# Kernel tuning notes

Measured on AMD Instinct MI355X. Metric: run time of the kernel, lower is better.

Reference implementation:

```python
import jax, jax.numpy as jnp
import numpy as np

LOW_THRESH, HIGH_THRESH = 0.1, 0.2   # kornia canny defaults
HYST_ITERS = 10                      # fixed-point hysteresis iterations (fixed for jit)


def _gaussian_kernel5(sigma=1.0):
    x = jnp.arange(5, dtype=jnp.float32) - 2.0
    g = jnp.exp(-0.5 * (x / sigma) ** 2)
    g = g / g.sum()
    return jnp.outer(g, g)  # [5,5]


def _conv2d(x, k):
    # x: [B,1,H,W]; k: [kh,kw]; reflect pad + VALID conv == SAME with reflect border
    kh, kw = k.shape
    xp = jnp.pad(x, ((0, 0), (0, 0), (kh // 2, kh // 2), (kw // 2, kw // 2)), mode="reflect")
    return jax.lax.conv_general_dilated(
        xp, k[None, None], (1, 1), "VALID",
        dimension_numbers=("NCHW", "OIHW", "NCHW"))


def _shift(x, dy, dx):
    # value of neighbor at (i+dy, j+dx), zero-padded border; x: [B,1,H,W]
    H, W = x.shape[2], x.shape[3]
    xp = jnp.pad(x, ((0, 0), (0, 0), (1, 1), (1, 1)))
    return xp[:, :, 1 + dy:1 + dy + H, 1 + dx:1 + dx + W]


def _canny_edges(img):
    # img: [B,3,H,W] in [0,1] -> binary edge map [B,1,H,W]
    gray = 0.299 * img[:, :1] + 0.587 * img[:, 1:2] + 0.114 * img[:, 2:3]
    blur = _conv2d(gray, _gaussian_kernel5())
    sobel_x = jnp.array([[-1., 0., 1.], [-2., 0., 2.], [-1., 0., 1.]], jnp.float32)
    gx = _conv2d(blur, sobel_x)
    gy = _conv2d(blur, sobel_x.T)
    mag = jnp.sqrt(gx * gx + gy * gy + 1e-12)
    ang = jnp.arctan2(gy, gx)

    # non-maximum suppression: quantize gradient direction to 4 bins (0/45/90/135 deg)
    b = jnp.mod(jnp.round(ang / (jnp.pi / 4.0)), 4).astype(jnp.int32)  # [B,1,H,W]
    n_pos = jnp.stack([_shift(mag, 0, 1), _shift(mag, 1, 1),
                       _shift(mag, 1, 0), _shift(mag, 1, -1)], axis=0)  # [4,B,1,H,W]
    n_neg = jnp.stack([_shift(mag, 0, -1), _shift(mag, -1, -1),
                       _shift(mag, -1, 0), _shift(mag, -1, 1)], axis=0)
    n1 = jnp.take_along_axis(n_pos, b[None], axis=0)[0]
    n2 = jnp.take_along_axis(n_neg, b[None], axis=0)[0]
    nms = jnp.where((mag >= n1) & (mag >= n2), mag, 0.0)

    # double threshold: strong=1.0, weak=0.5
    edges = jnp.where(nms >= HIGH_THRESH, 1.0,
                      jnp.where(nms >= LOW_THRESH, 0.5, 0.0))

    # hysteresis: weak pixels with a strong 8-neighbor become strong (iterated)
    def body(_, e):
        strong = (e == 1.0).astype(e.dtype)
        nb = jax.lax.reduce_window(strong, 0.0, jax.lax.max,
                                   (1, 1, 3, 3), (1, 1, 1, 1), "SAME")
        promoted = (e == 0.5) & (nb > 0.5)
        return jnp.where(promoted, 1.0, e)

    edges = jax.lax.fori_loop(0, HYST_ITERS, body, edges)
    return (edges == 1.0).astype(jnp.float32)


def setup_inputs() -> dict:
    key = jax.random.key(0)
    k1, k2 = jax.random.split(key)
    shape = (16, 3, 512, 512)
    return {"y_hat": jax.random.uniform(k1, shape, jnp.float32),
            "y": jax.random.uniform(k2, shape, jnp.float32)}


def reference(y_hat, y):
    y_hat_edges = _canny_edges(y_hat)
    y_edges = _canny_edges(y)
    return jnp.mean(jnp.abs(y_hat_edges - y_edges))  # F.l1_loss, mean reduction
```

## Files before the change

kernel.cpp:

```cpp
#include <hip/hip_runtime.h>
#include <math.h>

#define H 512
#define W 512
#define IMG (H*W)
#define NIMG 32

typedef unsigned long long u64;

__device__ __forceinline__ int reflect_idx(int i, int n) {
    if (i < 0) i = -i;
    if (i >= n) i = 2 * n - 2 - i;
    return i;
}

#define EBX 64
#define EBY 16

__global__ __launch_bounds__(512) void k_edges(const float* __restrict__ yhat,
                                               const float* __restrict__ yy,
                                               u64* __restrict__ strongP,
                                               u64* __restrict__ weakP) {
    __shared__ float sg[EBY + 8][EBX + 8 + 1];
    __shared__ float ht[EBY + 8][EBX + 4 + 1];
    __shared__ float sb[EBY + 4][EBX + 4 + 1];
    __shared__ float sm[EBY + 2][EBX + 2 + 1];

    const int n = blockIdx.z;
    const float* src = (n < 16) ? (yhat + (size_t)n * 3 * IMG)
                                : (yy + (size_t)(n - 16) * 3 * IMG);
    const int x0 = blockIdx.x * EBX;
    const int y0 = blockIdx.y * EBY;
    const int tid = threadIdx.y * EBX + threadIdx.x;

    const float w0 = 0.05448868454964294f, w1 = 0.24420134200323332f,
                w2 = 0.4026199468942475f;
    const float wk[5] = {w0, w1, w2, w1, w0};

    for (int idx = tid; idx < 24 * 72; idx += 512) {
        int sy = idx / 72, sx = idx % 72;
        int iy = reflect_idx(y0 - 4 + sy, H);
        int ix = reflect_idx(x0 - 4 + sx, W);
        float r = src[(size_t)iy * W + ix];
        float g = src[(size_t)IMG + (size_t)iy * W + ix];
        float b = src[(size_t)2 * IMG + (size_t)iy * W + ix];
        sg[sy][sx] = 0.299f * r + 0.587f * g + 0.114f * b;
    }
    __syncthreads();

    for (int idx = tid; idx < 24 * 68; idx += 512) {
        int sy = idx / 68, sx = idx % 68;
        float a = 0.f;
#pragma unroll
        for (int v = 0; v < 5; v++) a += wk[v] * sg[sy][sx + v];
        ht[sy][sx] = a;
    }
    __syncthreads();

    for (int idx = tid; idx < 20 * 68; idx += 512) {
        int sy = idx / 68, sx = idx % 68;
        float a = 0.f;
#pragma unroll
        for (int u = 0; u < 5; u++) a += wk[u] * ht[sy + u][sx];
        sb[sy][sx] = a;
    }
    __syncthreads();

    for (int idx = tid; idx < 18 * 66; idx += 512) {
        int my = idx / 66, mx = idx % 66;
        int iy = y0 - 1 + my, ix = x0 - 1 + mx;
        float m = 0.f;
        if (iy >= 0 && iy < H && ix >= 0 && ix < W) {
            float a00 = sb[my][mx],     a01 = sb[my][mx + 1],     a02 = sb[my][mx + 2];
            float a10 = sb[my + 1][mx],                           a12 = sb[my + 1][mx + 2];
            float a20 = sb[my + 2][mx], a21 = sb[my + 2][mx + 1], a22 = sb[my + 2][mx + 2];
            float gx = (a02 + 2.f * a12 + a22) - (a00 + 2.f * a10 + a20);
            float gy = (a20 + 2.f * a21 + a22) - (a00 + 2.f * a01 + a02);
            m = sqrtf(gx * gx + gy * gy + 1e-12f);
        }
        sm[my][mx] = m;
    }
    __syncthreads();

    const int tx = threadIdx.x;
#pragma unroll
    for (int half = 0; half < 2; half++) {
        const int ry = threadIdx.y + half * 8;
        float a00 = sb[ry + 1][tx + 1], a01 = sb[ry + 1][tx + 2], a02 = sb[ry + 1][tx + 3];
        float a10 = sb[ry + 2][tx + 1],                           a12 = sb[ry + 2][tx + 3];
        float a20 = sb[ry + 3][tx + 1], a21 = sb[ry + 3][tx + 2], a22 = sb[ry + 3][tx + 3];
        float gx = (a02 + 2.f * a12 + a22) - (a00 + 2.f * a10 + a20);
        float gy = (a20 + 2.f * a21 + a22) - (a00 + 2.f * a01 + a02);
        float mag = sm[ry + 1][tx + 1];

        float ax = fabsf(gx), ay = fabsf(gy);
        int dy, dx;
        if (ay <= 0.4142135623730951f * ax) { dy = 0; dx = 1; }
        else if (ay >= 2.414213562373095f * ax) { dy = 1; dx = 0; }
        else { dy = 1; dx = ((gx > 0.f) == (gy > 0.f)) ? 1 : -1; }

        float n1 = sm[ry + 1 + dy][tx + 1 + dx];
        float n2 = sm[ry + 1 - dy][tx + 1 - dx];
        float nms = (mag >= n1 && mag >= n2) ? mag : 0.f;

        u64 strong = __ballot(nms >= 0.2f);
        u64 weak   = __ballot(nms >= 0.1f);
        if (tx == 0) {
            size_t off = ((size_t)n * H + (y0 + ry)) * 8 + blockIdx.x;
            strongP[off] = strong;
            weakP[off] = weak;
        }
    }
}

__device__ __forceinline__ u64 ldw(const u64* p, int img, int y, int w, bool ok) {
    return (ok && w >= 0 && w < 8) ? p[((size_t)img * H + y) * 8 + w] : 0ULL;
}

__global__ __launch_bounds__(256) void k_hyst(const u64* __restrict__ strongP,
                                              const u64* __restrict__ weakP,
                                              unsigned int* __restrict__ partials) {
    __shared__ unsigned int part[4];
    const int wy = threadIdx.x >> 6;
    const int wave = blockIdx.x * 4 + wy;
    const int lane = threadIdx.x & 63;
    const int tile = wave & 255;
    const int pair = wave >> 8;
    const int tx0 = (tile & 15) * 32;
    const int ty0 = (tile >> 4) * 32;

    const int y = ty0 - 10 + lane;
    const bool rowok = (lane < 52) && (y >= 0) && (y < H);
    const int s = tx0 - 10;
    const int w0i = s >> 6;
    const int r = s & 63;

    const int imgA = pair, imgB = pair + 16;
    u64 sA, wA, sB, wB;
    {
        u64 lo, hi;
        lo = ldw(strongP, imgA, y, w0i, rowok); hi = ldw(strongP, imgA, y, w0i + 1, rowok);
        sA = (lo >> r) | (hi << (64 - r));
        lo = ldw(weakP, imgA, y, w0i, rowok);   hi = ldw(weakP, imgA, y, w0i + 1, rowok);
        wA = (lo >> r) | (hi << (64 - r));
        lo = ldw(strongP, imgB, y, w0i, rowok); hi = ldw(strongP, imgB, y, w0i + 1, rowok);
        sB = (lo >> r) | (hi << (64 - r));
        lo = ldw(weakP, imgB, y, w0i, rowok);   hi = ldw(weakP, imgB, y, w0i + 1, rowok);
        wB = (lo >> r) | (hi << (64 - r));
    }

#pragma unroll
    for (int it = 0; it < 10; it++) {
        u64 up = __shfl_up(sA, 1), dn = __shfl_down(sA, 1);
        u64 t = up | sA | dn;
        sA |= (t | (t << 1) | (t >> 1)) & wA;
        up = __shfl_up(sB, 1); dn = __shfl_down(sB, 1);
        t = up | sB | dn;
        sB |= (t | (t << 1) | (t >> 1)) & wB;
    }

    unsigned int c = 0;
    if (lane >= 10 && lane < 42) {
        const u64 mask = ((1ULL << 42) - (1ULL << 10));
        c = (unsigned int)__popcll((sA ^ sB) & mask);
    }
#pragma unroll
    for (int off = 32; off > 0; off >>= 1) c += __shfl_down(c, off);
    if (lane == 0) part[wy] = c;
    __syncthreads();
    if (threadIdx.x == 0)
        partials[blockIdx.x] = part[0] + part[1] + part[2] + part[3];
}

__global__ __launch_bounds__(256) void k_final(const unsigned int* __restrict__ partials,
                                               float* __restrict__ out) {
    __shared__ unsigned int part[4];
    unsigned int c = 0;
    for (int i = threadIdx.x; i < 1024; i += 256) c += partials[i];
#pragma unroll
    for (int off = 32; off > 0; off >>= 1) c += __shfl_down(c, off);
    const int lane = threadIdx.x & 63;
    const int wy = threadIdx.x >> 6;
    if (lane == 0) part[wy] = c;
    __syncthreads();
    if (threadIdx.x == 0)
        out[0] = (float)(part[0] + part[1] + part[2] + part[3]) * (1.0f / 4194304.0f);
}

extern "C" void kernel_launch(void* const* d_in, const int* in_sizes, int n_in,
                              void* d_out, int out_size, void* d_ws, size_t ws_size,
                              hipStream_t stream) {
    const float* yhat = (const float*)d_in[0];
    const float* yy = (const float*)d_in[1];

    u64* strongP = (u64*)d_ws;
    u64* weakP = strongP + (size_t)NIMG * H * 8;
    unsigned int* partials = (unsigned int*)(weakP + (size_t)NIMG * H * 8);

    dim3 eblk(EBX, 8);
    dim3 egrd(W / EBX, H / EBY, NIMG);
    k_edges<<<egrd, eblk, 0, stream>>>(yhat, yy, strongP, weakP);

    k_hyst<<<1024, 256, 0, stream>>>(strongP, weakP, partials);
    k_final<<<1, 256, 0, stream>>>(partials, (float*)d_out);
}
```

Before: 153.2 us.

## Fold Gaussian blur into separable Sobel filters and enlarge edge tile

Precomputes combined Gaussian*Sobel separable 1D kernels so gradients come from two separable passes instead of blur then Sobel, removing an intermediate stage and a sync. Doubles the row tile to 32 to cut halo overhead, reuses LDS by aliasing buffers, vectorises the horizontal pass with float4 reads, and stores a precomputed NMS neighbor offset per pixel. Floating-point results may differ slightly from blur-then-Sobel ordering, which can flip threshold decisions at the margins.

```diff
diff --git a/kernel.cpp b/kernel.cpp
--- a/kernel.cpp
+++ b/kernel.cpp
@@ -14,97 +14,111 @@
     return i;
 }
 
-#define EBX 64
-#define EBY 16
+#define S0 0.05448868454964294f
+#define S1 0.35317871110251920f
+#define S2 0.94551131545035710f
+#define S3 1.29364257779496160f
+#define A1 0.05448868454964294f
+#define A2 0.24420134200323332f
+#define A3 0.34813126234460456f
+
+#define TY 32
 
 __global__ __launch_bounds__(512) void k_edges(const float* __restrict__ yhat,
                                                const float* __restrict__ yy,
                                                u64* __restrict__ strongP,
                                                u64* __restrict__ weakP) {
-    __shared__ float sg[EBY + 8][EBX + 8 + 1];
-    __shared__ float ht[EBY + 8][EBX + 4 + 1];
-    __shared__ float sb[EBY + 4][EBX + 4 + 1];
-    __shared__ float sm[EBY + 2][EBX + 2 + 1];
+    __shared__ __align__(16) char lds[12768 + 22848];
+    float (*sg)[76] = (float (*)[76])lds;
+    float (*hxy)[68][2] = (float (*)[68][2])(lds + 12768);
+    float (*sm)[68] = (float (*)[68])lds;
+    unsigned char (*sbin)[68] = (unsigned char (*)[68])(lds + 9792);
 
     const int n = blockIdx.z;
     const float* src = (n < 16) ? (yhat + (size_t)n * 3 * IMG)
                                 : (yy + (size_t)(n - 16) * 3 * IMG);
-    const int x0 = blockIdx.x * EBX;
-    const int y0 = blockIdx.y * EBY;
-    const int tid = threadIdx.y * EBX + threadIdx.x;
-
-    const float w0 = 0.05448868454964294f, w1 = 0.24420134200323332f,
-                w2 = 0.4026199468942475f;
-    const float wk[5] = {w0, w1, w2, w1, w0};
-
-    for (int idx = tid; idx < 24 * 72; idx += 512) {
-        int sy = idx / 72, sx = idx % 72;
-        int iy = reflect_idx(y0 - 4 + sy, H);
-        int ix = reflect_idx(x0 - 4 + sx, W);
-        float r = src[(size_t)iy * W + ix];
-        float g = src[(size_t)IMG + (size_t)iy * W + ix];
-        float b = src[(size_t)2 * IMG + (size_t)iy * W + ix];
-        sg[sy][sx] = 0.299f * r + 0.587f * g + 0.114f * b;
-    }
-    __syncthreads();
-
-    for (int idx = tid; idx < 24 * 68; idx += 512) {
-        int sy = idx / 68, sx = idx % 68;
-        float a = 0.f;
-#pragma unroll
-        for (int v = 0; v < 5; v++) a += wk[v] * sg[sy][sx + v];
-        ht[sy][sx] = a;
-    }
-    __syncthreads();
-
-    for (int idx = tid; idx < 20 * 68; idx += 512) {
-        int sy = idx / 68, sx = idx % 68;
-        float a = 0.f;
-#pragma unroll
-        for (int u = 0; u < 5; u++) a += wk[u] * ht[sy + u][sx];
-        sb[sy][sx] = a;
-    }
-    __syncthreads();
-
-    for (int idx = tid; idx < 18 * 66; idx += 512) {
-        int my = idx / 66, mx = idx % 66;
-        int iy = y0 - 1 + my, ix = x0 - 1 + mx;
-        float m = 0.f;
-        if (iy >= 0 && iy < H && ix >= 0 && ix < W) {
-            float a00 = sb[my][mx],     a01 = sb[my][mx + 1],     a02 = sb[my][mx + 2];
-            float a10 = sb[my + 1][mx],                           a12 = sb[my + 1][mx + 2];
-            float a20 = sb[my + 2][mx], a21 = sb[my + 2][mx + 1], a22 = sb[my + 2][mx + 2];
-            float gx = (a02 + 2.f * a12 + a22) - (a00 + 2.f * a10 + a20);
-            float gy = (a20 + 2.f * a21 + a22) - (a00 + 2.f * a01 + a02);
-            m = sqrtf(gx * gx + gy * gy + 1e-12f);
-        }
-        sm[my][mx] = m;
-    }
-    __syncthreads();
-
-    const int tx = threadIdx.x;
-#pragma unroll
-    for (int half = 0; half < 2; half++) {
-        const int ry = threadIdx.y + half * 8;
-        float a00 = sb[ry + 1][tx + 1], a01 = sb[ry + 1][tx + 2], a02 = sb[ry + 1][tx + 3];
-        float a10 = sb[ry + 2][tx + 1],                           a12 = sb[ry + 2][tx + 3];
-        float a20 = sb[ry + 3][tx + 1], a21 = sb[ry + 3][tx + 2], a22 = sb[ry + 3][tx + 3];
-        float gx = (a02 + 2.f * a12 + a22) - (a00 + 2.f * a10 + a20);
-        float gy = (a20 + 2.f * a21 + a22) - (a00 + 2.f * a01 + a02);
-        float mag = sm[ry + 1][tx + 1];
-
-        float ax = fabsf(gx), ay = fabsf(gy);
-        int dy, dx;
-        if (ay <= 0.4142135623730951f * ax) { dy = 0; dx = 1; }
-        else if (ay >= 2.414213562373095f * ax) { dy = 1; dx = 0; }
-        else { dy = 1; dx = ((gx > 0.f) == (gy > 0.f)) ? 1 : -1; }
-
-        float n1 = sm[ry + 1 + dy][tx + 1 + dx];
-        float n2 = sm[ry + 1 - dy][tx + 1 - dx];
+    const int x0 = blockIdx.x * 64;
+    const int y0 = blockIdx.y * TY;
+    const int tx = threadIdx.x, ty = threadIdx.y;
+    const int tid = ty * 64 + tx;
+
+    const int ixA = reflect_idx(x0 - 4 + tx, W);
+    const int ixB = reflect_idx(x0 + 60 + tx, W);
+#pragma unroll
+    for (int k = 0; k < 6; k++) {
+        int sy = ty + 8 * k;
+        if (sy < 42) {
+            int iy = reflect_idx(y0 - 4 + sy, H);
+            const float* row = src + iy * W;
+            float r = row[ixA], g = row[IMG + ixA], b = row[2 * IMG + ixA];
+            sg[sy][tx] = 0.299f * r + 0.587f * g + 0.114f * b;
+            if (tx < 8) {
+                float r2 = row[ixB], g2 = row[IMG + ixB], b2 = row[2 * IMG + ixB];
+                sg[sy][64 + tx] = 0.299f * r2 + 0.587f * g2 + 0.114f * b2;
+            }
+        }
+    }
+    __syncthreads();
+
+    for (int t = tid; t < 714; t += 512) {
+        int sy = t / 17, g = t % 17;
+        const float4* p = (const float4*)&sg[sy][0];
+        float4 q0 = p[g], q1 = p[g + 1], q2 = p[g + 2];
+        float w[12] = {q0.x, q0.y, q0.z, q0.w, q1.x, q1.y, q1.z, q1.w,
+                       q2.x, q2.y, q2.z, q2.w};
+#pragma unroll
+        for (int j = 0; j < 4; j++) {
+            float hx = A3 * (w[j + 4] - w[j + 2]) + A2 * (w[j + 5] - w[j + 1])
+                     + A1 * (w[j + 6] - w[j + 0]);
+            float hy = S3 * w[j + 3] + S2 * (w[j + 4] + w[j + 2])
+                     + S1 * (w[j + 5] + w[j + 1]) + S0 * (w[j + 6] + w[j + 0]);
+            *(float2*)&hxy[sy][4 * g + j][0] = make_float2(hx, hy);
+        }
+    }
+    __syncthreads();
+
+    for (int t = tid; t < 594; t += 512) {
+        int rg = t / 66, c = t % 66;
+        float hx[10], hy[10];
+#pragma unroll
+        for (int i = 0; i < 10; i++) {
+            float2 v = *(const float2*)&hxy[4 * rg + i][c][0];
+            hx[i] = v.x; hy[i] = v.y;
+        }
+        int imgcol = x0 - 1 + c;
+        bool colok = (unsigned)imgcol < (unsigned)W;
+#pragma unroll
+        for (int j = 0; j < 4; j++) {
+            int my = 4 * rg + j;
+            float gx = S3 * hx[j + 3] + S2 * (hx[j + 4] + hx[j + 2])
+                     + S1 * (hx[j + 5] + hx[j + 1]) + S0 * (hx[j + 6] + hx[j + 0]);
+            float gy = A3 * (hy[j + 4] - hy[j + 2]) + A2 * (hy[j + 5] - hy[j + 1])
+                     + A1 * (hy[j + 6] - hy[j + 0]);
+            int imgrow = y0 - 1 + my;
+            bool ok = colok && ((unsigned)imgrow < (unsigned)H);
+            float m = ok ? sqrtf(gx * gx + gy * gy + 1e-12f) : 0.f;
+            sm[my][c] = m;
+            float ax = fabsf(gx), ay = fabsf(gy);
+            int d;
+            if (ay <= 0.4142135623730951f * ax) d = 1;
+            else if (ay >= 2.414213562373095f * ax) d = 68;
+            else d = ((gx > 0.f) == (gy > 0.f)) ? 69 : 67;
+            sbin[my][c] = (unsigned char)d;
+        }
+    }
+    __syncthreads();
+
+#pragma unroll
+    for (int k = 0; k < 4; k++) {
+        int ry = ty + 8 * k;
+        const float* cp = &sm[ry + 1][tx + 1];
+        float mag = cp[0];
+        int d = sbin[ry + 1][tx + 1];
+        float n1 = cp[d];
+        float n2 = cp[-d];
         float nms = (mag >= n1 && mag >= n2) ? mag : 0.f;
-
         u64 strong = __ballot(nms >= 0.2f);
-        u64 weak   = __ballot(nms >= 0.1f);
+        u64 weak = __ballot(nms >= 0.1f);
         if (tx == 0) {
             size_t off = ((size_t)n * H + (y0 + ry)) * 8 + blockIdx.x;
             strongP[off] = strong;
@@ -197,8 +211,8 @@
     u64* weakP = strongP + (size_t)NIMG * H * 8;
     unsigned int* partials = (unsigned int*)(weakP + (size_t)NIMG * H * 8);
 
-    dim3 eblk(EBX, 8);
-    dim3 egrd(W / EBX, H / EBY, NIMG);
+    dim3 eblk(64, 8);
+    dim3 egrd(W / 64, H / TY, NIMG);
     k_edges<<<egrd, eblk, 0, stream>>>(yhat, yy, strongP, weakP);
 
     k_hyst<<<1024, 256, 0, stream>>>(strongP, weakP, partials);
```

Result: no change. 155.9 us (+1.7%).

## Rewrite edge kernel as per-wave column strips with rolling registers and fused blur-Sobel

Applied to the files above, without the earlier changes.

Replaces the shared-memory tiled edge kernel with one wave per 56-column strip that streams rows down a 32-row band. Blur and Sobel are folded into separable 7-tap filters, and the neighbour taps are exchanged across lanes with ds_bpermute. Magnitude and direction for the last three rows are kept in registers for NMS. Squared magnitude is compared against squared thresholds so the sqrt is dropped. The bitmask layout moves to 10 strips of 56 bits, so the hysteresis kernel now stitches up to three words per row, and the halo columns mean extra recomputation.

```diff
diff --git a/kernel.cpp b/kernel.cpp
--- a/kernel.cpp
+++ b/kernel.cpp
@@ -5,6 +5,10 @@
 #define W 512
 #define IMG (H*W)
 #define NIMG 32
+#define NSTRIP 10
+#define SW 56
+#define RB 32
+#define NBAND 16
 
 typedef unsigned long long u64;
 
@@ -14,107 +18,103 @@
     return i;
 }
 
-#define EBX 64
-#define EBY 16
-
-__global__ __launch_bounds__(512) void k_edges(const float* __restrict__ yhat,
+__device__ __forceinline__ float bperm_f(int addr, float v) {
+    return __int_as_float(__builtin_amdgcn_ds_bpermute(addr, __float_as_int(v)));
+}
+
+#define S0 0.05448868454964294f
+#define S1 0.35317871110251920f
+#define S2 0.94551131545035710f
+#define S3 1.29364257779496160f
+#define A1 0.05448868454964294f
+#define A2 0.24420134200323332f
+#define A3 0.34813126234460456f
+
+__global__ __launch_bounds__(256) void k_edges(const float* __restrict__ yhat,
                                                const float* __restrict__ yy,
                                                u64* __restrict__ strongP,
                                                u64* __restrict__ weakP) {
-    __shared__ float sg[EBY + 8][EBX + 8 + 1];
-    __shared__ float ht[EBY + 8][EBX + 4 + 1];
-    __shared__ float sb[EBY + 4][EBX + 4 + 1];
-    __shared__ float sm[EBY + 2][EBX + 2 + 1];
-
-    const int n = blockIdx.z;
+    const int wid = blockIdx.x * 4 + (threadIdx.x >> 6);
+    const int lane = threadIdx.x & 63;
+    const int n = wid / (NSTRIP * NBAND);
+    const int rem = wid - n * (NSTRIP * NBAND);
+    const int s = rem >> 4;
+    const int band = rem & 15;
+    const int y0 = band * RB;
     const float* src = (n < 16) ? (yhat + (size_t)n * 3 * IMG)
                                 : (yy + (size_t)(n - 16) * 3 * IMG);
-    const int x0 = blockIdx.x * EBX;
-    const int y0 = blockIdx.y * EBY;
-    const int tid = threadIdx.y * EBX + threadIdx.x;
-
-    const float w0 = 0.05448868454964294f, w1 = 0.24420134200323332f,
-                w2 = 0.4026199468942475f;
-    const float wk[5] = {w0, w1, w2, w1, w0};
-
-    for (int idx = tid; idx < 24 * 72; idx += 512) {
-        int sy = idx / 72, sx = idx % 72;
-        int iy = reflect_idx(y0 - 4 + sy, H);
-        int ix = reflect_idx(x0 - 4 + sx, W);
-        float r = src[(size_t)iy * W + ix];
-        float g = src[(size_t)IMG + (size_t)iy * W + ix];
-        float b = src[(size_t)2 * IMG + (size_t)iy * W + ix];
-        sg[sy][sx] = 0.299f * r + 0.587f * g + 0.114f * b;
-    }
-    __syncthreads();
-
-    for (int idx = tid; idx < 24 * 68; idx += 512) {
-        int sy = idx / 68, sx = idx % 68;
-        float a = 0.f;
-#pragma unroll
-        for (int v = 0; v < 5; v++) a += wk[v] * sg[sy][sx + v];
-        ht[sy][sx] = a;
-    }
-    __syncthreads();
-
-    for (int idx = tid; idx < 20 * 68; idx += 512) {
-        int sy = idx / 68, sx = idx % 68;
-        float a = 0.f;
-#pragma unroll
-        for (int u = 0; u < 5; u++) a += wk[u] * ht[sy + u][sx];
-        sb[sy][sx] = a;
-    }
-    __syncthreads();
-
-    for (int idx = tid; idx < 18 * 66; idx += 512) {
-        int my = idx / 66, mx = idx % 66;
-        int iy = y0 - 1 + my, ix = x0 - 1 + mx;
-        float m = 0.f;
-        if (iy >= 0 && iy < H && ix >= 0 && ix < W) {
-            float a00 = sb[my][mx],     a01 = sb[my][mx + 1],     a02 = sb[my][mx + 2];
-            float a10 = sb[my + 1][mx],                           a12 = sb[my + 1][mx + 2];
-            float a20 = sb[my + 2][mx], a21 = sb[my + 2][mx + 1], a22 = sb[my + 2][mx + 2];
-            float gx = (a02 + 2.f * a12 + a22) - (a00 + 2.f * a10 + a20);
-            float gy = (a20 + 2.f * a21 + a22) - (a00 + 2.f * a01 + a02);
-            m = sqrtf(gx * gx + gy * gy + 1e-12f);
-        }
-        sm[my][mx] = m;
-    }
-    __syncthreads();
-
-    const int tx = threadIdx.x;
-#pragma unroll
-    for (int half = 0; half < 2; half++) {
-        const int ry = threadIdx.y + half * 8;
-        float a00 = sb[ry + 1][tx + 1], a01 = sb[ry + 1][tx + 2], a02 = sb[ry + 1][tx + 3];
-        float a10 = sb[ry + 2][tx + 1],                           a12 = sb[ry + 2][tx + 3];
-        float a20 = sb[ry + 3][tx + 1], a21 = sb[ry + 3][tx + 2], a22 = sb[ry + 3][tx + 3];
-        float gx = (a02 + 2.f * a12 + a22) - (a00 + 2.f * a10 + a20);
-        float gy = (a20 + 2.f * a21 + a22) - (a00 + 2.f * a01 + a02);
-        float mag = sm[ry + 1][tx + 1];
-
-        float ax = fabsf(gx), ay = fabsf(gy);
-        int dy, dx;
-        if (ay <= 0.4142135623730951f * ax) { dy = 0; dx = 1; }
-        else if (ay >= 2.414213562373095f * ax) { dy = 1; dx = 0; }
-        else { dy = 1; dx = ((gx > 0.f) == (gy > 0.f)) ? 1 : -1; }
-
-        float n1 = sm[ry + 1 + dy][tx + 1 + dx];
-        float n2 = sm[ry + 1 - dy][tx + 1 - dx];
-        float nms = (mag >= n1 && mag >= n2) ? mag : 0.f;
-
-        u64 strong = __ballot(nms >= 0.2f);
-        u64 weak   = __ballot(nms >= 0.1f);
-        if (tx == 0) {
-            size_t off = ((size_t)n * H + (y0 + ry)) * 8 + blockIdx.x;
-            strongP[off] = strong;
-            weakP[off] = weak;
-        }
-    }
-}
-
-__device__ __forceinline__ u64 ldw(const u64* p, int img, int y, int w, bool ok) {
-    return (ok && w >= 0 && w < 8) ? p[((size_t)img * H + y) * 8 + w] : 0ULL;
+
+    const int c = s * SW - 4 + lane;
+    const int cx = reflect_idx(c, W);
+    const bool colok = ((unsigned)c < (unsigned)W);
+    const u64 omask = (s == 9) ? 0xFFull : 0x00FFFFFFFFFFFFFFull;
+
+    const int aM3 = ((lane - 3) << 2), aM2 = ((lane - 2) << 2), aM1 = ((lane - 1) << 2);
+    const int aP1 = ((lane + 1) << 2), aP2 = ((lane + 2) << 2), aP3 = ((lane + 3) << 2);
+
+    float hx[7], hy[7];
+    float mPrev = 0.f, mPrevL = 0.f, mPrevR = 0.f;
+    float mCur = 0.f, mCurL = 0.f, mCurR = 0.f;
+    int dCur = 0, dNew = 0;
+
+    u64 outBase = ((size_t)n * NSTRIP + s) * H;
+
+    for (int i = 0; i < RB + 8; i++) {
+#pragma unroll
+        for (int j = 0; j < 6; j++) { hx[j] = hx[j + 1]; hy[j] = hy[j + 1]; }
+        {
+            int gr = reflect_idx(y0 - 4 + i, H);
+            const float* p = src + (size_t)gr * W + cx;
+            float g = 0.299f * p[0] + 0.587f * p[IMG] + 0.114f * p[2 * IMG];
+            float gm1 = bperm_f(aM1, g), gp1 = bperm_f(aP1, g);
+            float gm2 = bperm_f(aM2, g), gp2 = bperm_f(aP2, g);
+            float gm3 = bperm_f(aM3, g), gp3 = bperm_f(aP3, g);
+            hx[6] = A3 * (gp1 - gm1) + A2 * (gp2 - gm2) + A1 * (gp3 - gm3);
+            hy[6] = S3 * g + S2 * (gp1 + gm1) + S1 * (gp2 + gm2) + S0 * (gp3 + gm3);
+        }
+
+        float mNew = 0.f, mNewL = 0.f, mNewR = 0.f;
+        if (i >= 6) {
+            float gx = S3 * hx[3] + S2 * (hx[4] + hx[2])
+                     + S1 * (hx[5] + hx[1]) + S0 * (hx[6] + hx[0]);
+            float gy = A3 * (hy[4] - hy[2]) + A2 * (hy[5] - hy[1])
+                     + A1 * (hy[6] - hy[0]);
+            int mr = y0 - 7 + i;
+            bool ok = colok && ((unsigned)mr < (unsigned)H);
+            mNew = ok ? (gx * gx + gy * gy + 1e-12f) : 0.f;
+            mNewL = bperm_f(aM1, mNew);
+            mNewR = bperm_f(aP1, mNew);
+            float ax = fabsf(gx), ay = fabsf(gy);
+            dNew = (ay <= 0.4142135623730951f * ax) ? 0
+                 : (ay >= 2.414213562373095f * ax) ? 2
+                 : (((gx > 0.f) == (gy > 0.f)) ? 1 : 3);
+        }
+
+        if (i >= 8) {
+            float n1 = (dCur == 0) ? mCurR : (dCur == 1) ? mNewR
+                     : (dCur == 2) ? mNew : mNewL;
+            float n2 = (dCur == 0) ? mCurL : (dCur == 1) ? mPrevL
+                     : (dCur == 2) ? mPrev : mPrevR;
+            bool okn = (mCur >= n1) && (mCur >= n2);
+            u64 bs = __ballot(okn && (mCur >= 0.04f));
+            u64 bw = __ballot(okn && (mCur >= 0.01f));
+            if (lane == 0) {
+                int t = y0 - 8 + i;
+                strongP[outBase + t] = (bs >> 4) & omask;
+                weakP[outBase + t] = (bw >> 4) & omask;
+            }
+        }
+
+        if (i >= 6) {
+            mPrev = mCur; mPrevL = mCurL; mPrevR = mCurR;
+            mCur = mNew; mCurL = mNewL; mCurR = mNewR;
+            dCur = dNew;
+        }
+    }
+}
+
+__device__ __forceinline__ u64 ldw10(const u64* p, int img, int y, int q, bool ok) {
+    return (ok && q >= 0 && q < NSTRIP) ? p[((size_t)img * NSTRIP + q) * H + y] : 0ULL;
 }
 
 __global__ __launch_bounds__(256) void k_hyst(const u64* __restrict__ strongP,
@@ -131,22 +131,35 @@
 
     const int y = ty0 - 10 + lane;
     const bool rowok = (lane < 52) && (y >= 0) && (y < H);
-    const int s = tx0 - 10;
-    const int w0i = s >> 6;
-    const int r = s & 63;
+    const int yc = rowok ? y : 0;
+
+    const int x = tx0 - 10;
+    const int q0 = (x < 0) ? -1 : (x / 56);
+    const int r = x - 56 * q0;
+    const int sh1 = 56 - r;
+    const bool need3 = (r > 48);
+    const int sh2 = 112 - r;
 
     const int imgA = pair, imgB = pair + 16;
     u64 sA, wA, sB, wB;
     {
-        u64 lo, hi;
-        lo = ldw(strongP, imgA, y, w0i, rowok); hi = ldw(strongP, imgA, y, w0i + 1, rowok);
-        sA = (lo >> r) | (hi << (64 - r));
-        lo = ldw(weakP, imgA, y, w0i, rowok);   hi = ldw(weakP, imgA, y, w0i + 1, rowok);
-        wA = (lo >> r) | (hi << (64 - r));
-        lo = ldw(strongP, imgB, y, w0i, rowok); hi = ldw(strongP, imgB, y, w0i + 1, rowok);
-        sB = (lo >> r) | (hi << (64 - r));
-        lo = ldw(weakP, imgB, y, w0i, rowok);   hi = ldw(weakP, imgB, y, w0i + 1, rowok);
-        wB = (lo >> r) | (hi << (64 - r));
+        u64 w0, w1, w2;
+        w0 = ldw10(strongP, imgA, yc, q0, rowok);
+        w1 = ldw10(strongP, imgA, yc, q0 + 1, rowok);
+        w2 = need3 ? ldw10(strongP, imgA, yc, q0 + 2, rowok) : 0ULL;
+        sA = (w0 >> r) | (w1 << sh1) | (need3 ? (w2 << sh2) : 0ULL);
+        w0 = ldw10(weakP, imgA, yc, q0, rowok);
+        w1 = ldw10(weakP, imgA, yc, q0 + 1, rowok);
+        w2 = need3 ? ldw10(weakP, imgA, yc, q0 + 2, rowok) : 0ULL;
+        wA = (w0 >> r) | (w1 << sh1) | (need3 ? (w2 << sh2) : 0ULL);
+        w0 = ldw10(strongP, imgB, yc, q0, rowok);
+        w1 = ldw10(strongP, imgB, yc, q0 + 1, rowok);
+        w2 = need3 ? ldw10(strongP, imgB, yc, q0 + 2, rowok) : 0ULL;
+        sB = (w0 >> r) | (w1 << sh1) | (need3 ? (w2 << sh2) : 0ULL);
+        w0 = ldw10(weakP, imgB, yc, q0, rowok);
+        w1 = ldw10(weakP, imgB, yc, q0 + 1, rowok);
+        w2 = need3 ? ldw10(weakP, imgB, yc, q0 + 2, rowok) : 0ULL;
+        wB = (w0 >> r) | (w1 << sh1) | (need3 ? (w2 << sh2) : 0ULL);
     }
 
 #pragma unroll
@@ -159,14 +172,14 @@
         sB |= (t | (t << 1) | (t >> 1)) & wB;
     }
 
-    unsigned int c = 0;
+    unsigned int cgt = 0;
     if (lane >= 10 && lane < 42) {
         const u64 mask = ((1ULL << 42) - (1ULL << 10));
-        c = (unsigned int)__popcll((sA ^ sB) & mask);
-    }
-#pragma unroll
-    for (int off = 32; off > 0; off >>= 1) c += __shfl_down(c, off);
-    if (lane == 0) part[wy] = c;
+        cgt = (unsigned int)__popcll((sA ^ sB) & mask);
+    }
+#pragma unroll
+    for (int off = 32; off > 0; off >>= 1) cgt += __shfl_down(cgt, off);
+    if (lane == 0) part[wy] = cgt;
     __syncthreads();
     if (threadIdx.x == 0)
         partials[blockIdx.x] = part[0] + part[1] + part[2] + part[3];
@@ -194,12 +207,10 @@
     const float* yy = (const float*)d_in[1];
 
     u64* strongP = (u64*)d_ws;
-    u64* weakP = strongP + (size_t)NIMG * H * 8;
-    unsigned int* partials = (unsigned int*)(weakP + (size_t)NIMG * H * 8);
-
-    dim3 eblk(EBX, 8);
-    dim3 egrd(W / EBX, H / EBY, NIMG);
-    k_edges<<<egrd, eblk, 0, stream>>>(yhat, yy, strongP, weakP);
+    u64* weakP = strongP + (size_t)NIMG * NSTRIP * H;
+    unsigned int* partials = (unsigned int*)(weakP + (size_t)NIMG * NSTRIP * H);
+
+    k_edges<<<1280, 256, 0, stream>>>(yhat, yy, strongP, weakP);
 
     k_hyst<<<1024, 256, 0, stream>>>(strongP, weakP, partials);
     k_final<<<1, 256, 0, stream>>>(partials, (float*)d_out);
```

New measurement: 146.6 us. 4.3% less time.
